# Kernel optimization log

Measured on AMD Instinct MI355X. Metric: run time of the kernel, lower is better.

## Reference

```python
import jax, jax.numpy as jnp
import numpy as np

N = 10000      # nodes
E = 320000     # edges (before self-loops)
D = 256        # d_model
DC = 128       # d_content = d_model // 2
L = 3          # num_layers
K = 4096       # nodes_of_interest
LN_EPS = 1e-5


def setup_inputs() -> dict:
    key = jax.random.key(0)
    ks = jax.random.split(key, 7)
    x = jax.random.normal(ks[0], (N, D), dtype=jnp.float32)
    edge_index = jax.random.randint(ks[1], (2, E), 0, N)
    nodes_of_interest = jax.random.randint(ks[2], (K,), 0, N)
    # per-layer linear weights (stacked over layers)
    Wc = jax.random.normal(ks[3], (L, DC, DC), dtype=jnp.float32) * (1.0 / np.sqrt(DC))
    bc = jnp.zeros((L, DC), dtype=jnp.float32)
    Wp = jax.random.normal(ks[4], (L, DC, DC), dtype=jnp.float32) * (1.0 / np.sqrt(DC))
    bp = jnp.zeros((L, DC), dtype=jnp.float32)
    gamma = jnp.ones((L, D), dtype=jnp.float32)
    beta = jnp.zeros((L, D), dtype=jnp.float32)
    return {"x": x, "edge_index": edge_index, "nodes_of_interest": nodes_of_interest,
            "Wc": Wc, "bc": bc, "Wp": Wp, "bp": bp, "gamma": gamma, "beta": beta}


def _layernorm(h, g, b):
    mu = jnp.mean(h, axis=-1, keepdims=True)
    var = jnp.mean((h - mu) ** 2, axis=-1, keepdims=True)
    return (h - mu) * jax.lax.rsqrt(var + LN_EPS) * g + b


def reference(x, edge_index, nodes_of_interest, Wc, bc, Wp, bp, gamma, beta):
    n = x.shape[0]
    loops = jnp.arange(n)
    # add self-loops (PyG add_self_loops): done per conv in torch but identical each layer
    row = jnp.concatenate([edge_index[0], loops])  # source j
    col = jnp.concatenate([edge_index[1], loops])  # target i
    # symmetric-ish normalization: degree counted over row only (as in source)
    deg = jax.ops.segment_sum(jnp.ones_like(row, dtype=x.dtype), row, num_segments=n)
    dis = deg ** -0.5
    norm = dis[row] * dis[col]  # [E+N]

    def conv(h, l):
        hc = h[:, :DC] @ Wc[l].T + bc[l]
        hp = h[:, DC:] @ Wp[l].T + bp[l]
        ht = jnp.concatenate([hc, hp], axis=-1)
        msg = norm[:, None] * ht[row]                      # gather + normalize
        return jax.ops.segment_sum(msg, col, num_segments=n)  # scatter-add

    for l in range(L - 1):
        x = x + jax.nn.relu(_layernorm(conv(x, l), gamma[l], beta[l]))
    x = x + _layernorm(conv(x, L - 1), gamma[L - 1], beta[L - 1])
    return x[nodes_of_interest]
```

## Files before the change

### kernel.cpp

```cpp
#include <hip/hip_runtime.h>
#include <hip/hip_bf16.h>

#define DMODEL 256
#define DCH 128
#define NLAYER 3
#define LN_EPS 1e-5f

typedef float f32x4 __attribute__((ext_vector_type(4)));
typedef short s16x8 __attribute__((ext_vector_type(8)));

__device__ __forceinline__ unsigned short f2bf(float f) {
  unsigned int u = __float_as_uint(f);
  unsigned int r = (u + 0x7FFF + ((u >> 16) & 1)) >> 16;
  return (unsigned short)r;
}

__device__ __forceinline__ unsigned int pk2bf(float x, float y) {
  return ((unsigned int)f2bf(y) << 16) | f2bf(x);
}


__global__ __launch_bounds__(256) void hist_kernel(const int* __restrict__ row,
    const int* __restrict__ col, int* cnt_row, int* cnt_col, int E) {
  int e = blockIdx.x * 256 + threadIdx.x;
  if (e < E) {
    atomicAdd(&cnt_row[row[e]], 1);
    atomicAdd(&cnt_col[col[e]], 1);
  }
}

__global__ __launch_bounds__(256) void scan_dis_kernel(
    const int* __restrict__ cnt_col, const int* __restrict__ cnt_row,
    int* __restrict__ indptr, int* __restrict__ cursor,
    float* __restrict__ dis, int N, int E) {
  int t = threadIdx.x;
  for (int i = t; i < N; i += 256) dis[i] = rsqrtf((float)(cnt_row[i] + 1));

  const int PER = (N + 255) / 256;
  int start = t * PER;
  int sum = 0;
  for (int k = 0; k < PER; ++k) {
    int i = start + k;
    if (i < N) sum += cnt_col[i];
  }
  int lane = t & 63, wid = t >> 6;
  int inc = sum;
#pragma unroll
  for (int off = 1; off < 64; off <<= 1) {
    int v = __shfl_up(inc, off);
    if (lane >= off) inc += v;
  }
  __shared__ int wsum[4];
  if (lane == 63) wsum[wid] = inc;
  __syncthreads();
  int woff = 0;
  for (int w = 0; w < wid; ++w) woff += wsum[w];
  int run = woff + inc - sum;
  for (int k = 0; k < PER; ++k) {
    int i = start + k;
    if (i < N) {
      indptr[i] = run;
      cursor[i] = run;
      run += cnt_col[i];
    }
  }
  if (t == 255) indptr[N] = E;
}

__global__ __launch_bounds__(256) void fill_kernel(const int* __restrict__ row,
    const int* __restrict__ col, int* cursor, int* __restrict__ idx, int E) {
  int e = blockIdx.x * 256 + threadIdx.x;
  if (e < E) {
    int pos = atomicAdd(&cursor[col[e]], 1);
    idx[pos] = row[e];
  }
}


__global__ __launch_bounds__(256) void gemm_mfma_kernel(const float* __restrict__ x,
    const float* __restrict__ Wc, const float* __restrict__ bc,
    const float* __restrict__ Wp, const float* __restrict__ bp,
    unsigned short* __restrict__ ht, int layer, int Nn) {
  int h = blockIdx.y;
  const float* __restrict__ W = (h ? Wp : Wc) + (size_t)layer * DCH * DCH;
  const float* __restrict__ b = (h ? bp : bc) + (size_t)layer * DCH;
  int i0 = blockIdx.x * 32;
  int t = threadIdx.x;
  int w = t >> 6;
  int lane = t & 63;
  int mt = w & 1;
  int cg = w >> 1;
  int lrow = lane & 15;
  int kgrp = lane >> 4;

  int arow = i0 + mt * 16 + lrow;
  int arow_c = min(arow, Nn - 1);
  const float* ap = x + (size_t)arow_c * DMODEL + h * DCH + kgrp * 8;

  int bcol[4];
  const float* bp_[4];
  f32x4 acc[4];
#pragma unroll
  for (int nt = 0; nt < 4; ++nt) {
    bcol[nt] = cg * 64 + nt * 16 + lrow;
    bp_[nt] = W + bcol[nt] * DCH + kgrp * 8;
    float bias = b[bcol[nt]];
    acc[nt] = (f32x4){bias, bias, bias, bias};
  }

  union U8 { s16x8 v; unsigned int u[4]; };

#pragma unroll
  for (int kt = 0; kt < 4; ++kt) {
    float4 a0 = *(const float4*)(ap + kt * 32);
    float4 a1 = *(const float4*)(ap + kt * 32 + 4);
    U8 af;
    af.u[0] = pk2bf(a0.x, a0.y);
    af.u[1] = pk2bf(a0.z, a0.w);
    af.u[2] = pk2bf(a1.x, a1.y);
    af.u[3] = pk2bf(a1.z, a1.w);
#pragma unroll
    for (int nt = 0; nt < 4; ++nt) {
      float4 b0 = *(const float4*)(bp_[nt] + kt * 32);
      float4 b1 = *(const float4*)(bp_[nt] + kt * 32 + 4);
      U8 bf;
      bf.u[0] = pk2bf(b0.x, b0.y);
      bf.u[1] = pk2bf(b0.z, b0.w);
      bf.u[2] = pk2bf(b1.x, b1.y);
      bf.u[3] = pk2bf(b1.z, b1.w);
      acc[nt] = __builtin_amdgcn_mfma_f32_16x16x32_bf16(af.v, bf.v, acc[nt], 0, 0, 0);
    }
  }

#pragma unroll
  for (int nt = 0; nt < 4; ++nt) {
#pragma unroll
    for (int j = 0; j < 4; ++j) {
      int gi = i0 + mt * 16 + kgrp * 4 + j;
      if (gi < Nn) ht[(size_t)gi * DMODEL + h * DCH + bcol[nt]] = f2bf(acc[nt][j]);
    }
  }
}


__device__ __forceinline__ void bf2x(unsigned int u, float w, float& a0, float& a1) {
  a0 += w * __uint_as_float(u << 16);
  a1 += w * __uint_as_float(u & 0xFFFF0000u);
}

__global__ __launch_bounds__(128) void agg_kernel(const float* __restrict__ xin,
    const unsigned short* __restrict__ ht, float* __restrict__ xout,
    const float* __restrict__ dis, const int* __restrict__ indptr,
    const int* __restrict__ idx, const float* __restrict__ gamma,
    const float* __restrict__ beta, const int* __restrict__ noi,
    int use_noi, int relu) {
  int b = blockIdx.x;
  int i = use_noi ? noi[b] : b;
  int t = threadIdx.x;
  float di = dis[i];
  size_t rbase = (size_t)i * DMODEL + 2 * t;

  unsigned int us = *(const unsigned int*)&ht[rbase];
  float w2s = di * di;
  float acc0 = w2s * __uint_as_float(us << 16);
  float acc1 = w2s * __uint_as_float(us & 0xFFFF0000u);

  int s = indptr[i], e = indptr[i + 1];
  __shared__ int s_src[128];
  __shared__ float s_w[128];
  for (int base = s; base < e; base += 128) {
    int n = min(128, e - base);
    __syncthreads();
    if (t < n) {
      int sr = idx[base + t];
      s_src[t] = sr;
      s_w[t] = dis[sr] * di;
    }
    __syncthreads();
    int j = 0;
    for (; j + 4 <= n; j += 4) {
      int  q0 = s_src[j], q1 = s_src[j + 1], q2 = s_src[j + 2], q3 = s_src[j + 3];
      float w0 = s_w[j], w1 = s_w[j + 1], w2 = s_w[j + 2], w3 = s_w[j + 3];
      unsigned int u0 = *(const unsigned int*)&ht[(size_t)q0 * DMODEL + 2 * t];
      unsigned int u1 = *(const unsigned int*)&ht[(size_t)q1 * DMODEL + 2 * t];
      unsigned int u2 = *(const unsigned int*)&ht[(size_t)q2 * DMODEL + 2 * t];
      unsigned int u3 = *(const unsigned int*)&ht[(size_t)q3 * DMODEL + 2 * t];
      bf2x(u0, w0, acc0, acc1);
      bf2x(u1, w1, acc0, acc1);
      bf2x(u2, w2, acc0, acc1);
      bf2x(u3, w3, acc0, acc1);
    }
    for (; j < n; ++j) {
      unsigned int u = *(const unsigned int*)&ht[(size_t)s_src[j] * DMODEL + 2 * t];
      bf2x(u, s_w[j], acc0, acc1);
    }
  }

  float v1 = acc0 + acc1, v2 = acc0 * acc0 + acc1 * acc1;
#pragma unroll
  for (int o = 32; o > 0; o >>= 1) {
    v1 += __shfl_down(v1, o);
    v2 += __shfl_down(v2, o);
  }
  __shared__ float w1s[2], w2ss[2];
  int wid = t >> 6, lane = t & 63;
  if (lane == 0) { w1s[wid] = v1; w2ss[wid] = v2; }
  __syncthreads();
  float s1 = w1s[0] + w1s[1];
  float s2 = w2ss[0] + w2ss[1];
  float mu = s1 * (1.0f / DMODEL);
  float var = s2 * (1.0f / DMODEL) - mu * mu;
  float rs = rsqrtf(var + LN_EPS);
  float2 g = *(const float2*)&gamma[2 * t];
  float2 bb = *(const float2*)&beta[2 * t];
  float y0 = (acc0 - mu) * rs * g.x + bb.x;
  float y1 = (acc1 - mu) * rs * g.y + bb.y;
  if (relu) { y0 = fmaxf(y0, 0.f); y1 = fmaxf(y1, 0.f); }
  float2 xi = *(const float2*)&xin[rbase];
  size_t ob = (size_t)(use_noi ? b : i) * DMODEL + 2 * t;
  *(float2*)&xout[ob] = make_float2(xi.x + y0, xi.y + y1);
}

extern "C" void kernel_launch(void* const* d_in, const int* in_sizes, int n_in,
                              void* d_out, int out_size, void* d_ws, size_t ws_size,
                              hipStream_t stream) {
  const float* x     = (const float*)d_in[0];
  const int*   edges = (const int*)d_in[1];
  const int*   noi   = (const int*)d_in[2];
  const float* Wc    = (const float*)d_in[3];
  const float* bc    = (const float*)d_in[4];
  const float* Wp    = (const float*)d_in[5];
  const float* bp    = (const float*)d_in[6];
  const float* gamma = (const float*)d_in[7];
  const float* beta  = (const float*)d_in[8];

  int N = in_sizes[0] / DMODEL;
  int E = in_sizes[1] / 2;
  int K = in_sizes[2];
  const int* row = edges;
  const int* col = edges + E;

  char* base = (char*)d_ws;
  size_t off = 0;
  auto alloc = [&](size_t bytes) -> void* {
    void* p = base + off;
    off += (bytes + 255) & ~(size_t)255;
    return p;
  };

  float*          xA     = (float*)alloc((size_t)N * DMODEL * 4);
  float*          xB     = (float*)alloc((size_t)N * DMODEL * 4);
  unsigned short* htb    = (unsigned short*)alloc((size_t)N * DMODEL * 2);
  float*          dis    = (float*)alloc((size_t)N * 4);
  int*            cnt    = (int*)alloc((size_t)2 * N * 4);
  int*            indptr = (int*)alloc((size_t)(N + 1) * 4);
  int*            cursor = (int*)alloc((size_t)N * 4);
  int*            idx    = (int*)alloc((size_t)E * 4);

  hipMemsetAsync(cnt, 0, (size_t)2 * N * 4, stream);

  int eb = (E + 255) / 256;
  hist_kernel<<<eb, 256, 0, stream>>>(row, col, cnt, cnt + N, E);
  scan_dis_kernel<<<1, 256, 0, stream>>>(cnt + N, cnt, indptr, cursor, dis, N, E);
  fill_kernel<<<eb, 256, 0, stream>>>(row, col, cursor, idx, E);

  const float* cur_in = x;
  float* bufs[2] = {xA, xB};
  for (int l = 0; l < NLAYER; ++l) {
    dim3 ggrid((N + 31) / 32, 2);
    gemm_mfma_kernel<<<ggrid, 256, 0, stream>>>(cur_in, Wc, bc, Wp, bp, htb, l, N);
    if (l < NLAYER - 1) {
      agg_kernel<<<N, 128, 0, stream>>>(cur_in, htb, bufs[l & 1], dis, indptr, idx,
                                        gamma + (size_t)l * DMODEL,
                                        beta + (size_t)l * DMODEL,
                                        nullptr, 0, 1);
      cur_in = bufs[l & 1];
    } else {
      agg_kernel<<<K, 128, 0, stream>>>(cur_in, htb, (float*)d_out, dis, indptr, idx,
                                        gamma + (size_t)l * DMODEL,
                                        beta + (size_t)l * DMODEL,
                                        noi, 1, 0);
    }
  }
}
```

Baseline: 278.3 us.

## Aggregate before transform and fuse GEMM with LayerNorm epilogue

Reorders each layer to aggregate raw bf16 node features first, then apply the linear transform. The bias is scaled by the per-node weight sum, which is valid because aggregation is linear. The transform GEMM now fuses LayerNorm, ReLU and the residual, and emits a bf16 copy of the next layer's input. Inputs and weights are pre-converted to bf16 in the histogram kernel, and aggregation uses one wave per node with shuffles instead of shared memory. This removes the separate GEMM pass and lets the last layer's GEMM run only on the nodes of interest. In exchange it uses extra bf16 buffers and rounds the aggregated sum to bf16 before the GEMM, which adds precision risk.

```diff
diff --git a/kernel.cpp b/kernel.cpp
--- a/kernel.cpp
+++ b/kernel.cpp
@@ -1,5 +1,4 @@
 #include <hip/hip_runtime.h>
-#include <hip/hip_bf16.h>
 
 #define DMODEL 256
 #define DCH 128
@@ -14,18 +13,38 @@
   unsigned int r = (u + 0x7FFF + ((u >> 16) & 1)) >> 16;
   return (unsigned short)r;
 }
-
 __device__ __forceinline__ unsigned int pk2bf(float x, float y) {
   return ((unsigned int)f2bf(y) << 16) | f2bf(x);
 }
-
-
-__global__ __launch_bounds__(256) void hist_kernel(const int* __restrict__ row,
-    const int* __restrict__ col, int* cnt_row, int* cnt_col, int E) {
-  int e = blockIdx.x * 256 + threadIdx.x;
-  if (e < E) {
-    atomicAdd(&cnt_row[row[e]], 1);
-    atomicAdd(&cnt_col[col[e]], 1);
+__device__ __forceinline__ float bflo(unsigned int u) { return __uint_as_float(u << 16); }
+__device__ __forceinline__ float bfhi(unsigned int u) { return __uint_as_float(u & 0xFFFF0000u); }
+
+__global__ __launch_bounds__(256) void hist_cvt_kernel(
+    const int* __restrict__ row, const int* __restrict__ col,
+    int* cnt_row, int* cnt_col, int E,
+    const float* __restrict__ x, unsigned short* __restrict__ xbf, int nx8,
+    const float* __restrict__ Wc, unsigned short* __restrict__ Wcb,
+    const float* __restrict__ Wp, unsigned short* __restrict__ Wpb, int nw8) {
+  int tid = blockIdx.x * 256 + threadIdx.x;
+  if (tid < E) {
+    atomicAdd(&cnt_row[row[tid]], 1);
+    atomicAdd(&cnt_col[col[tid]], 1);
+  }
+  if (tid < nx8) {
+    float4 a = *(const float4*)&x[tid * 8];
+    float4 b = *(const float4*)&x[tid * 8 + 4];
+    uint4 o = {pk2bf(a.x, a.y), pk2bf(a.z, a.w), pk2bf(b.x, b.y), pk2bf(b.z, b.w)};
+    *(uint4*)&xbf[tid * 8] = o;
+  }
+  if (tid < nw8) {
+    float4 a = *(const float4*)&Wc[tid * 8];
+    float4 b = *(const float4*)&Wc[tid * 8 + 4];
+    uint4 o = {pk2bf(a.x, a.y), pk2bf(a.z, a.w), pk2bf(b.x, b.y), pk2bf(b.z, b.w)};
+    *(uint4*)&Wcb[tid * 8] = o;
+    a = *(const float4*)&Wp[tid * 8];
+    b = *(const float4*)&Wp[tid * 8 + 4];
+    uint4 o2 = {pk2bf(a.x, a.y), pk2bf(a.z, a.w), pk2bf(b.x, b.y), pk2bf(b.z, b.w)};
+    *(uint4*)&Wpb[tid * 8] = o2;
   }
 }
 
@@ -35,7 +54,6 @@
     float* __restrict__ dis, int N, int E) {
   int t = threadIdx.x;
   for (int i = t; i < N; i += 256) dis[i] = rsqrtf((float)(cnt_row[i] + 1));
-
   const int PER = (N + 255) / 256;
   int start = t * PER;
   int sum = 0;
@@ -76,149 +94,164 @@
   }
 }
 
-
-__global__ __launch_bounds__(256) void gemm_mfma_kernel(const float* __restrict__ x,
-    const float* __restrict__ Wc, const float* __restrict__ bc,
-    const float* __restrict__ Wp, const float* __restrict__ bp,
-    unsigned short* __restrict__ ht, int layer, int Nn) {
-  int h = blockIdx.y;
-  const float* __restrict__ W = (h ? Wp : Wc) + (size_t)layer * DCH * DCH;
-  const float* __restrict__ b = (h ? bp : bc) + (size_t)layer * DCH;
-  int i0 = blockIdx.x * 32;
-  int t = threadIdx.x;
-  int w = t >> 6;
-  int lane = t & 63;
-  int mt = w & 1;
-  int cg = w >> 1;
-  int lrow = lane & 15;
-  int kgrp = lane >> 4;
-
-  int arow = i0 + mt * 16 + lrow;
-  int arow_c = min(arow, Nn - 1);
-  const float* ap = x + (size_t)arow_c * DMODEL + h * DCH + kgrp * 8;
-
-  int bcol[4];
-  const float* bp_[4];
-  f32x4 acc[4];
-#pragma unroll
-  for (int nt = 0; nt < 4; ++nt) {
-    bcol[nt] = cg * 64 + nt * 16 + lrow;
-    bp_[nt] = W + bcol[nt] * DCH + kgrp * 8;
-    float bias = b[bcol[nt]];
-    acc[nt] = (f32x4){bias, bias, bias, bias};
-  }
-
-  union U8 { s16x8 v; unsigned int u[4]; };
-
-#pragma unroll
-  for (int kt = 0; kt < 4; ++kt) {
-    float4 a0 = *(const float4*)(ap + kt * 32);
-    float4 a1 = *(const float4*)(ap + kt * 32 + 4);
-    U8 af;
-    af.u[0] = pk2bf(a0.x, a0.y);
-    af.u[1] = pk2bf(a0.z, a0.w);
-    af.u[2] = pk2bf(a1.x, a1.y);
-    af.u[3] = pk2bf(a1.z, a1.w);
-#pragma unroll
-    for (int nt = 0; nt < 4; ++nt) {
-      float4 b0 = *(const float4*)(bp_[nt] + kt * 32);
-      float4 b1 = *(const float4*)(bp_[nt] + kt * 32 + 4);
-      U8 bf;
-      bf.u[0] = pk2bf(b0.x, b0.y);
-      bf.u[1] = pk2bf(b0.z, b0.w);
-      bf.u[2] = pk2bf(b1.x, b1.y);
-      bf.u[3] = pk2bf(b1.z, b1.w);
-      acc[nt] = __builtin_amdgcn_mfma_f32_16x16x32_bf16(af.v, bf.v, acc[nt], 0, 0, 0);
-    }
-  }
-
-#pragma unroll
-  for (int nt = 0; nt < 4; ++nt) {
-#pragma unroll
-    for (int j = 0; j < 4; ++j) {
-      int gi = i0 + mt * 16 + kgrp * 4 + j;
-      if (gi < Nn) ht[(size_t)gi * DMODEL + h * DCH + bcol[nt]] = f2bf(acc[nt][j]);
-    }
-  }
-}
-
-
-__device__ __forceinline__ void bf2x(unsigned int u, float w, float& a0, float& a1) {
-  a0 += w * __uint_as_float(u << 16);
-  a1 += w * __uint_as_float(u & 0xFFFF0000u);
-}
-
-__global__ __launch_bounds__(128) void agg_kernel(const float* __restrict__ xin,
-    const unsigned short* __restrict__ ht, float* __restrict__ xout,
-    const float* __restrict__ dis, const int* __restrict__ indptr,
-    const int* __restrict__ idx, const float* __restrict__ gamma,
-    const float* __restrict__ beta, const int* __restrict__ noi,
-    int use_noi, int relu) {
-  int b = blockIdx.x;
-  int i = use_noi ? noi[b] : b;
-  int t = threadIdx.x;
+__global__ __launch_bounds__(256) void agg_kernel(
+    const unsigned short* __restrict__ xbf, unsigned short* __restrict__ S,
+    float* __restrict__ swt, const float* __restrict__ dis,
+    const int* __restrict__ indptr, const int* __restrict__ idx,
+    const int* __restrict__ noi, int use_noi, int R) {
+  int wave = threadIdx.x >> 6, lane = threadIdx.x & 63;
+  int r = blockIdx.x * 4 + wave;
+  int rc = min(r, R - 1);
+  int i = use_noi ? noi[rc] : rc;
   float di = dis[i];
-  size_t rbase = (size_t)i * DMODEL + 2 * t;
-
-  unsigned int us = *(const unsigned int*)&ht[rbase];
-  float w2s = di * di;
-  float acc0 = w2s * __uint_as_float(us << 16);
-  float acc1 = w2s * __uint_as_float(us & 0xFFFF0000u);
+  float di2 = di * di;
+
+  uint2 u = *(const uint2*)(xbf + (size_t)i * DMODEL + lane * 4);
+  float a0 = di2 * bflo(u.x), a1 = di2 * bfhi(u.x);
+  float a2 = di2 * bflo(u.y), a3 = di2 * bfhi(u.y);
 
   int s = indptr[i], e = indptr[i + 1];
-  __shared__ int s_src[128];
-  __shared__ float s_w[128];
-  for (int base = s; base < e; base += 128) {
-    int n = min(128, e - base);
-    __syncthreads();
-    if (t < n) {
-      int sr = idx[base + t];
-      s_src[t] = sr;
-      s_w[t] = dis[sr] * di;
-    }
-    __syncthreads();
+  float sw = 0.f;
+  for (int base = s; base < e; base += 64) {
+    int n = min(64, e - base);
+    int sr = 0;
+    float w = 0.f;
+    if (lane < n) {
+      sr = idx[base + lane];
+      w = dis[sr] * di;
+    }
     int j = 0;
     for (; j + 4 <= n; j += 4) {
-      int  q0 = s_src[j], q1 = s_src[j + 1], q2 = s_src[j + 2], q3 = s_src[j + 3];
-      float w0 = s_w[j], w1 = s_w[j + 1], w2 = s_w[j + 2], w3 = s_w[j + 3];
-      unsigned int u0 = *(const unsigned int*)&ht[(size_t)q0 * DMODEL + 2 * t];
-      unsigned int u1 = *(const unsigned int*)&ht[(size_t)q1 * DMODEL + 2 * t];
-      unsigned int u2 = *(const unsigned int*)&ht[(size_t)q2 * DMODEL + 2 * t];
-      unsigned int u3 = *(const unsigned int*)&ht[(size_t)q3 * DMODEL + 2 * t];
-      bf2x(u0, w0, acc0, acc1);
-      bf2x(u1, w1, acc0, acc1);
-      bf2x(u2, w2, acc0, acc1);
-      bf2x(u3, w3, acc0, acc1);
+      int s0 = __shfl(sr, j), s1 = __shfl(sr, j + 1), s2 = __shfl(sr, j + 2), s3 = __shfl(sr, j + 3);
+      float w0 = __shfl(w, j), w1 = __shfl(w, j + 1), w2 = __shfl(w, j + 2), w3 = __shfl(w, j + 3);
+      uint2 u0 = *(const uint2*)(xbf + (size_t)s0 * DMODEL + lane * 4);
+      uint2 u1 = *(const uint2*)(xbf + (size_t)s1 * DMODEL + lane * 4);
+      uint2 u2 = *(const uint2*)(xbf + (size_t)s2 * DMODEL + lane * 4);
+      uint2 u3 = *(const uint2*)(xbf + (size_t)s3 * DMODEL + lane * 4);
+      a0 += w0 * bflo(u0.x); a1 += w0 * bfhi(u0.x); a2 += w0 * bflo(u0.y); a3 += w0 * bfhi(u0.y);
+      a0 += w1 * bflo(u1.x); a1 += w1 * bfhi(u1.x); a2 += w1 * bflo(u1.y); a3 += w1 * bfhi(u1.y);
+      a0 += w2 * bflo(u2.x); a1 += w2 * bfhi(u2.x); a2 += w2 * bflo(u2.y); a3 += w2 * bfhi(u2.y);
+      a0 += w3 * bflo(u3.x); a1 += w3 * bfhi(u3.x); a2 += w3 * bflo(u3.y); a3 += w3 * bfhi(u3.y);
+      sw += w0 + w1 + w2 + w3;
     }
     for (; j < n; ++j) {
-      unsigned int u = *(const unsigned int*)&ht[(size_t)s_src[j] * DMODEL + 2 * t];
-      bf2x(u, s_w[j], acc0, acc1);
-    }
-  }
-
-  float v1 = acc0 + acc1, v2 = acc0 * acc0 + acc1 * acc1;
-#pragma unroll
-  for (int o = 32; o > 0; o >>= 1) {
-    v1 += __shfl_down(v1, o);
-    v2 += __shfl_down(v2, o);
-  }
-  __shared__ float w1s[2], w2ss[2];
-  int wid = t >> 6, lane = t & 63;
-  if (lane == 0) { w1s[wid] = v1; w2ss[wid] = v2; }
+      int sj = __shfl(sr, j);
+      float wj = __shfl(w, j);
+      uint2 uu = *(const uint2*)(xbf + (size_t)sj * DMODEL + lane * 4);
+      a0 += wj * bflo(uu.x); a1 += wj * bfhi(uu.x); a2 += wj * bflo(uu.y); a3 += wj * bfhi(uu.y);
+      sw += wj;
+    }
+  }
+  if (r < R) {
+    uint2 o = {pk2bf(a0, a1), pk2bf(a2, a3)};
+    *(uint2*)(S + (size_t)r * DMODEL + lane * 4) = o;
+    if (lane == 0) swt[r] = di2 + sw;
+  }
+}
+
+__global__ __launch_bounds__(512) void xform_kernel(
+    const unsigned short* __restrict__ S, const float* __restrict__ swt,
+    const unsigned short* __restrict__ Wcb, const unsigned short* __restrict__ Wpb,
+    const float* __restrict__ bc, const float* __restrict__ bp,
+    const float* __restrict__ gamma, const float* __restrict__ beta,
+    const float* __restrict__ xin, const int* __restrict__ noi,
+    float* __restrict__ xout, unsigned short* __restrict__ xbf_out,
+    int use_noi, int relu, int R) {
+  int t = threadIdx.x;
+  int w = t >> 6, lane = t & 63;
+  int mt = w & 1, cq = w >> 1;
+  int h = cq >> 1, cgg = cq & 1;
+  int lrow = lane & 15, kgrp = lane >> 4;
+  int r0 = blockIdx.x * 32;
+
+  int arow = r0 + mt * 16 + lrow;
+  int arow_c = min(arow, R - 1);
+  const unsigned short* ap = S + (size_t)arow_c * DMODEL + h * DCH + kgrp * 8;
+  const unsigned short* Wh = h ? Wpb : Wcb;
+  const float* bh = h ? bp : bc;
+
+  int orow0 = mt * 16 + kgrp * 4;
+  float sj[4];
+#pragma unroll
+  for (int j = 0; j < 4; ++j) sj[j] = swt[min(r0 + orow0 + j, R - 1)];
+
+  int colw[4];
+  const unsigned short* bpw[4];
+  f32x4 acc[4];
+#pragma unroll
+  for (int nt = 0; nt < 4; ++nt) {
+    colw[nt] = cgg * 64 + nt * 16 + lrow;
+    bpw[nt] = Wh + (size_t)colw[nt] * DCH + kgrp * 8;
+    float bias = bh[colw[nt]];
+    acc[nt] = (f32x4){bias * sj[0], bias * sj[1], bias * sj[2], bias * sj[3]};
+  }
+
+  union U8 { s16x8 v; uint4 q; };
+#pragma unroll
+  for (int kt = 0; kt < 4; ++kt) {
+    U8 af;
+    af.q = *(const uint4*)(ap + kt * 32);
+#pragma unroll
+    for (int nt = 0; nt < 4; ++nt) {
+      U8 bf;
+      bf.q = *(const uint4*)(bpw[nt] + kt * 32);
+      acc[nt] = __builtin_amdgcn_mfma_f32_16x16x32_bf16(af.v, bf.v, acc[nt], 0, 0, 0);
+    }
+  }
+
+  float p1[4], p2[4];
+#pragma unroll
+  for (int j = 0; j < 4; ++j) {
+    p1[j] = acc[0][j] + acc[1][j] + acc[2][j] + acc[3][j];
+    p2[j] = acc[0][j] * acc[0][j] + acc[1][j] * acc[1][j] +
+            acc[2][j] * acc[2][j] + acc[3][j] * acc[3][j];
+  }
+#pragma unroll
+  for (int off = 8; off > 0; off >>= 1) {
+#pragma unroll
+    for (int j = 0; j < 4; ++j) {
+      p1[j] += __shfl_down(p1[j], off, 16);
+      p2[j] += __shfl_down(p2[j], off, 16);
+    }
+  }
+  __shared__ float red1[32][4], red2[32][4];
+  __shared__ float muS[32], rsS[32];
+  if (lrow == 0) {
+#pragma unroll
+    for (int j = 0; j < 4; ++j) {
+      red1[orow0 + j][cq] = p1[j];
+      red2[orow0 + j][cq] = p2[j];
+    }
+  }
   __syncthreads();
-  float s1 = w1s[0] + w1s[1];
-  float s2 = w2ss[0] + w2ss[1];
-  float mu = s1 * (1.0f / DMODEL);
-  float var = s2 * (1.0f / DMODEL) - mu * mu;
-  float rs = rsqrtf(var + LN_EPS);
-  float2 g = *(const float2*)&gamma[2 * t];
-  float2 bb = *(const float2*)&beta[2 * t];
-  float y0 = (acc0 - mu) * rs * g.x + bb.x;
-  float y1 = (acc1 - mu) * rs * g.y + bb.y;
-  if (relu) { y0 = fmaxf(y0, 0.f); y1 = fmaxf(y1, 0.f); }
-  float2 xi = *(const float2*)&xin[rbase];
-  size_t ob = (size_t)(use_noi ? b : i) * DMODEL + 2 * t;
-  *(float2*)&xout[ob] = make_float2(xi.x + y0, xi.y + y1);
+  if (t < 32) {
+    float s1 = red1[t][0] + red1[t][1] + red1[t][2] + red1[t][3];
+    float s2 = red2[t][0] + red2[t][1] + red2[t][2] + red2[t][3];
+    float mu = s1 * (1.0f / DMODEL);
+    float var = s2 * (1.0f / DMODEL) - mu * mu;
+    muS[t] = mu;
+    rsS[t] = rsqrtf(var + LN_EPS);
+  }
+  __syncthreads();
+
+#pragma unroll
+  for (int nt = 0; nt < 4; ++nt) {
+    int col = h * DCH + colw[nt];
+    float g = gamma[col], bt = beta[col];
+#pragma unroll
+    for (int j = 0; j < 4; ++j) {
+      int rr = orow0 + j;
+      int grow = r0 + rr;
+      if (grow < R) {
+        float y = (acc[nt][j] - muS[rr]) * rsS[rr] * g + bt;
+        if (relu) y = fmaxf(y, 0.f);
+        int node = use_noi ? noi[grow] : grow;
+        float o = xin[(size_t)node * DMODEL + col] + y;
+        xout[(size_t)grow * DMODEL + col] = o;
+        if (xbf_out) xbf_out[(size_t)grow * DMODEL + col] = f2bf(o);
+      }
+    }
+  }
 }
 
 extern "C" void kernel_launch(void* const* d_in, const int* in_sizes, int n_in,
@@ -237,6 +270,7 @@
   int N = in_sizes[0] / DMODEL;
   int E = in_sizes[1] / 2;
   int K = in_sizes[2];
+  int nwElem = in_sizes[3];
   const int* row = edges;
   const int* col = edges + E;
 
@@ -248,9 +282,15 @@
     return p;
   };
 
+  unsigned short* xbf0   = (unsigned short*)alloc((size_t)N * DMODEL * 2);
+  unsigned short* xbfA   = (unsigned short*)alloc((size_t)N * DMODEL * 2);
+  unsigned short* xbfB   = (unsigned short*)alloc((size_t)N * DMODEL * 2);
+  unsigned short* Sb     = (unsigned short*)alloc((size_t)N * DMODEL * 2);
   float*          xA     = (float*)alloc((size_t)N * DMODEL * 4);
   float*          xB     = (float*)alloc((size_t)N * DMODEL * 4);
-  unsigned short* htb    = (unsigned short*)alloc((size_t)N * DMODEL * 2);
+  unsigned short* Wcb    = (unsigned short*)alloc((size_t)nwElem * 2);
+  unsigned short* Wpb    = (unsigned short*)alloc((size_t)nwElem * 2);
+  float*          swt    = (float*)alloc((size_t)N * 4);
   float*          dis    = (float*)alloc((size_t)N * 4);
   int*            cnt    = (int*)alloc((size_t)2 * N * 4);
   int*            indptr = (int*)alloc((size_t)(N + 1) * 4);
@@ -259,27 +299,24 @@
 
   hipMemsetAsync(cnt, 0, (size_t)2 * N * 4, stream);
 
-  int eb = (E + 255) / 256;
-  hist_kernel<<<eb, 256, 0, stream>>>(row, col, cnt, cnt + N, E);
+  int nx8 = (N * DMODEL) / 8;
+  int nw8 = nwElem / 8;
+  int mx = E > nx8 ? E : nx8;
+  if (nw8 > mx) mx = nw8;
+  hist_cvt_kernel<<<(mx + 255) / 256, 256, 0, stream>>>(
+      row, col, cnt, cnt + N, E, x, xbf0, nx8, Wc, Wcb, Wp, Wpb, nw8);
   scan_dis_kernel<<<1, 256, 0, stream>>>(cnt + N, cnt, indptr, cursor, dis, N, E);
-  fill_kernel<<<eb, 256, 0, stream>>>(row, col, cursor, idx, E);
-
-  const float* cur_in = x;
-  float* bufs[2] = {xA, xB};
-  for (int l = 0; l < NLAYER; ++l) {
-    dim3 ggrid((N + 31) / 32, 2);
-    gemm_mfma_kernel<<<ggrid, 256, 0, stream>>>(cur_in, Wc, bc, Wp, bp, htb, l, N);
-    if (l < NLAYER - 1) {
-      agg_kernel<<<N, 128, 0, stream>>>(cur_in, htb, bufs[l & 1], dis, indptr, idx,
-                                        gamma + (size_t)l * DMODEL,
-                                        beta + (size_t)l * DMODEL,
-                                        nullptr, 0, 1);
-      cur_in = bufs[l & 1];
-    } else {
-      agg_kernel<<<K, 128, 0, stream>>>(cur_in, htb, (float*)d_out, dis, indptr, idx,
-                                        gamma + (size_t)l * DMODEL,
-                                        beta + (size_t)l * DMODEL,
-                                        noi, 1, 0);
-    }
-  }
-}
+  fill_kernel<<<(E + 255) / 256, 256, 0, stream>>>(row, col, cursor, idx, E);
+
+  agg_kernel<<<(N + 3) / 4, 256, 0, stream>>>(xbf0, Sb, swt, dis, indptr, idx, nullptr, 0, N);
+  xform_kernel<<<(N + 31) / 32, 512, 0, stream>>>(
+      Sb, swt, Wcb, Wpb, bc, bp, gamma, beta, x, nullptr, xA, xbfA, 0, 1, N);
+  agg_kernel<<<(N + 3) / 4, 256, 0, stream>>>(xbfA, Sb, swt, dis, indptr, idx, nullptr, 0, N);
+  xform_kernel<<<(N + 31) / 32, 512, 0, stream>>>(
+      Sb, swt, Wcb + (size_t)DCH * DCH, Wpb + (size_t)DCH * DCH, bc + DCH, bp + DCH,
+      gamma + DMODEL, beta + DMODEL, xA, nullptr, xB, xbfB, 0, 1, N);
+  agg_kernel<<<(K + 3) / 4, 256, 0, stream>>>(xbfB, Sb, swt, dis, indptr, idx, noi, 1, K);
+  xform_kernel<<<(K + 31) / 32, 512, 0, stream>>>(
+      Sb, swt, Wcb + (size_t)2 * DCH * DCH, Wpb + (size_t)2 * DCH * DCH, bc + 2 * DCH, bp + 2 * DCH,
+      gamma + 2 * DMODEL, beta + 2 * DMODEL, xB, noi, (float*)d_out, nullptr, 1, 0, K);
+}
```

Measured after the change: 265.5 us. -4.6%, faster.
